# Kernel tuning notes

Hardware: AMD Instinct MI355X
Metric: run time of the kernel (lower is better)

The kernel has to match this reference:

```python
import jax, jax.numpy as jnp
import numpy as np


def setup_inputs() -> dict:
    key = jax.random.key(0)
    k1, k2 = jax.random.split(key)
    B, N, M = 8, 4096, 4096
    xyz1 = jax.random.normal(k1, (B, N, 3), dtype=jnp.float32)
    xyz2 = jax.random.normal(k2, (B, M, 3), dtype=jnp.float32)
    return {"xyz1": xyz1, "xyz2": xyz2}


def _chamfer_sq_dists(xyz1, xyz2):
    # Squared euclidean all-pairs distances via ||a||^2 + ||b||^2 - 2 a.b
    # xyz1: [B,N,3], xyz2: [B,M,3]
    n1 = jnp.sum(xyz1 * xyz1, axis=-1)              # [B,N]
    n2 = jnp.sum(xyz2 * xyz2, axis=-1)              # [B,M]
    dots = jnp.einsum('bnd,bmd->bnm', xyz1, xyz2)   # [B,N,M]
    d2 = n1[:, :, None] + n2[:, None, :] - 2.0 * dots
    dist1 = jnp.min(d2, axis=2)                     # [B,N] min over xyz2
    dist2 = jnp.min(d2, axis=1)                     # [B,M] min over xyz1
    return dist1, dist2


def reference(xyz1, xyz2):
    dist1, dist2 = _chamfer_sq_dists(xyz1, xyz2)
    return jnp.mean(dist1) + jnp.mean(dist2)
```

## Files before the change

kernel.cpp:

```cpp
#include <hip/hip_runtime.h>

typedef float f32x16 __attribute__((ext_vector_type(16)));
typedef short bf16x8 __attribute__((ext_vector_type(8)));

#define BLOCK 256
#define NPTS 4096
#define SEGS 32
#define CHUNK 256
#define NCHUNK (NPTS / CHUNK)
#define SUBS (CHUNK / 32)

__device__ inline unsigned int f2bf(float x) {
    unsigned int u = __float_as_uint(x);
    return (u + 0x7FFFu + ((u >> 16) & 1)) >> 16;
}
__device__ inline float bf2f(unsigned int b) { return __uint_as_float(b << 16); }
__device__ inline unsigned int pk2(unsigned int lo, unsigned int hi) {
    return (hi << 16) | (lo & 0xFFFFu);
}

__global__ __launch_bounds__(BLOCK) void chamfer_fused(
    const float* __restrict__ x1, const float* __restrict__ x2,
    int Bc, float inv1, float inv2, float* __restrict__ out) {
    __shared__ uint4 lds[2][2][CHUNK];
    __shared__ float wslot[128];
    __shared__ float red[4];

    int tid = threadIdx.x;
    int lane = tid & 63, widx = tid >> 6;
    int l31 = lane & 31, blk = lane >> 5;

    int bid = blockIdx.x;
    int seg = bid % SEGS;
    int bd = bid / SEGS;
    int dir = (bd >= Bc) ? 1 : 0;
    int b = dir ? bd - Bc : bd;
    const float* own = dir ? x2 : x1;
    const float* oth = dir ? x1 : x2;
    float inv = dir ? inv2 : inv1;

    int row0 = seg * 128 + widx * 32;

    bf16x8 afA;
    {
        const float* p = own + ((size_t)b * NPTS + row0 + l31) * 3;
        float x = p[0], y = p[1], z = p[2];
        float w = fmaf(z, z, fmaf(y, y, x * x));
        unsigned int hx = f2bf(x), hy = f2bf(y), hz = f2bf(z);
        unsigned int lx = f2bf(x - bf2f(hx)), ly = f2bf(y - bf2f(hy)), lz = f2bf(z - bf2f(hz));
        unsigned int ax = f2bf(-2.f * bf2f(hx)), ay = f2bf(-2.f * bf2f(hy)), az = f2bf(-2.f * bf2f(hz));
        unsigned int bx = f2bf(-2.f * bf2f(lx)), by = f2bf(-2.f * bf2f(ly)), bz = f2bf(-2.f * bf2f(lz));
        const unsigned int one = 0x3F80u;
        uint4 A0 = make_uint4(pk2(ax, ay), pk2(az, bx), pk2(by, bz), pk2(ax, ay));
        uint4 A1 = make_uint4(pk2(az, one), pk2(one, 0u), 0u, 0u);
        uint4 af4 = blk ? A1 : A0;
        afA = *(const bf16x8*)&af4;
        if (!blk) wslot[widx * 32 + l31] = w;
    }

    const float* os = oth + (size_t)b * NPTS * 3;
    {
        const float* q = os + (size_t)tid * 3;
        float x = q[0], y = q[1], z = q[2];
        float w = fmaf(z, z, fmaf(y, y, x * x));
        unsigned int hx = f2bf(x), hy = f2bf(y), hz = f2bf(z);
        unsigned int lx = f2bf(x - bf2f(hx)), ly = f2bf(y - bf2f(hy)), lz = f2bf(z - bf2f(hz));
        unsigned int hw = f2bf(w), lw = f2bf(w - bf2f(hw));
        lds[0][0][tid] = make_uint4(pk2(hx, hy), pk2(hz, hx), pk2(hy, hz), pk2(lx, ly));
        lds[0][1][tid] = make_uint4(pk2(lz, hw), pk2(lw, 0u), 0u, 0u);
    }
    __syncthreads();

    f32x16 run;
#pragma unroll
    for (int r = 0; r < 16; ++r) run[r] = 3.0e38f;

    f32x16 zero = {};
    for (int c = 0; c < NCHUNK; ++c) {
        int cur = c & 1;
        float nx, ny, nz;
        if (c + 1 < NCHUNK) {
            const float* q = os + (size_t)((c + 1) * CHUNK + tid) * 3;
            nx = q[0]; ny = q[1]; nz = q[2];
        }
        const uint4* lp = lds[cur][blk];
#pragma unroll
        for (int s = 0; s < SUBS; s += 2) {
            bf16x8 bf0 = *(const bf16x8*)(lp + s * 32 + l31);
            bf16x8 bf1 = *(const bf16x8*)(lp + (s + 1) * 32 + l31);
            f32x16 acc0 = __builtin_amdgcn_mfma_f32_32x32x16_bf16(afA, bf0, zero, 0, 0, 0);
            f32x16 acc1 = __builtin_amdgcn_mfma_f32_32x32x16_bf16(afA, bf1, zero, 0, 0, 0);
#pragma unroll
            for (int r = 0; r < 16; ++r)
                run[r] = fminf(run[r], fminf(acc0[r], acc1[r]));
        }
        if (c + 1 < NCHUNK) {
            float w = fmaf(nz, nz, fmaf(ny, ny, nx * nx));
            unsigned int hx = f2bf(nx), hy = f2bf(ny), hz = f2bf(nz);
            unsigned int lx = f2bf(nx - bf2f(hx)), ly = f2bf(ny - bf2f(hy)), lz = f2bf(nz - bf2f(hz));
            unsigned int hw = f2bf(w), lw = f2bf(w - bf2f(hw));
            lds[cur ^ 1][0][tid] = make_uint4(pk2(hx, hy), pk2(hz, hx), pk2(hy, hz), pk2(lx, ly));
            lds[cur ^ 1][1][tid] = make_uint4(pk2(lz, hw), pk2(lw, 0u), 0u, 0u);
        }
        __syncthreads();
    }

#pragma unroll
    for (int m = 1; m <= 16; m <<= 1)
#pragma unroll
        for (int r = 0; r < 16; ++r)
            run[r] = fminf(run[r], __shfl_xor(run[r], m, 64));

    float contrib = 0.0f;
    if (l31 == 0) {
#pragma unroll
        for (int r = 0; r < 16; ++r) {
            int lrow = (r & 3) + 8 * (r >> 2) + 4 * blk;
            contrib += run[r] + wslot[widx * 32 + lrow];
        }
    }
    contrib += __shfl_xor(contrib, 32, 64);
    if (lane == 0) red[widx] = contrib * inv;
    __syncthreads();
    if (tid == 0) atomicAdd(out, red[0] + red[1] + red[2] + red[3]);
}

__global__ __launch_bounds__(BLOCK) void chamfer_direct(
    const float* __restrict__ x1, const float* __restrict__ x2,
    int Npts, int Mpts, float inv1, float inv2, float* __restrict__ out) {
    int dir = blockIdx.z;
    const float* own = dir ? x2 : x1;
    const float* oth = dir ? x1 : x2;
    int np = dir ? Mpts : Npts;
    int mp = dir ? Npts : Mpts;
    float scale = dir ? inv2 : inv1;

    int bpb = np / BLOCK;
    int b = blockIdx.x / bpb;
    int i = (blockIdx.x % bpb) * BLOCK + threadIdx.x;

    const float* pp = own + ((size_t)b * np + i) * 3;
    float px = pp[0], py = pp[1], pz = pp[2];
    const float* o = oth + (size_t)b * mp * 3;

    float best = 3.0e38f;
#pragma unroll 4
    for (int j = 0; j < mp; ++j) {
        float dx = px - o[3 * j + 0];
        float dy = py - o[3 * j + 1];
        float dz = pz - o[3 * j + 2];
        float d2 = fmaf(dz, dz, fmaf(dy, dy, dx * dx));
        best = fminf(best, d2);
    }
    float s = best * scale;
    for (int off = 32; off; off >>= 1) s += __shfl_down(s, off, 64);
    __shared__ float red[BLOCK / 64];
    int lane = threadIdx.x & 63, wid = threadIdx.x >> 6;
    if (!lane) red[wid] = s;
    __syncthreads();
    if (!threadIdx.x) atomicAdd(out, red[0] + red[1] + red[2] + red[3]);
}

extern "C" void kernel_launch(void* const* d_in, const int* in_sizes, int n_in,
                              void* d_out, int out_size, void* d_ws, size_t ws_size,
                              hipStream_t stream) {
    const float* xyz1 = (const float*)d_in[0];
    const float* xyz2 = (const float*)d_in[1];
    float* out = (float*)d_out;

    const int Bc = in_sizes[0] / (3 * NPTS);
    const int n1 = Bc * NPTS;
    const int n2 = Bc * NPTS;
    bool okShape = Bc >= 1 && in_sizes[0] == Bc * 3 * NPTS && in_sizes[1] == in_sizes[0];

    hipMemsetAsync(d_out, 0, sizeof(float), stream);

    if (okShape) {
        chamfer_fused<<<Bc * 2 * SEGS, BLOCK, 0, stream>>>(
            xyz1, xyz2, Bc, 1.0f / (float)n1, 1.0f / (float)n2, out);
    } else {
        dim3 grid((in_sizes[0] / 3 / NPTS) * (NPTS / BLOCK), 1, 2);
        chamfer_direct<<<grid, BLOCK, 0, stream>>>(xyz1, xyz2, NPTS, NPTS,
                                                   1.0f / (float)n1, 1.0f / (float)n2, out);
    }
}
```

Before: 38.21 us.

## Precompute packed bf16 point fragments in a separate kernel and halve block size

Adds a pack kernel that converts every point once into hi/lo bf16 MFMA operand fragments and squared norms in workspace. It also zeroes the output, which replaces the memset. The main MFMA kernel then streams the prepacked B fragments straight into LDS instead of having every block redo the split-bf16 conversion for all 4096 points. Blocks shrink to 128 threads and twice as many segments run, so occupancy stays about the same while the grid grows. In exchange there is an extra kernel launch, and each block now reads about 32 bytes per point from L2 instead of 12.

```diff
diff --git a/kernel.cpp b/kernel.cpp
--- a/kernel.cpp
+++ b/kernel.cpp
@@ -3,9 +3,9 @@
 typedef float f32x16 __attribute__((ext_vector_type(16)));
 typedef short bf16x8 __attribute__((ext_vector_type(8)));
 
-#define BLOCK 256
+#define BLOCK 128
 #define NPTS 4096
-#define SEGS 32
+#define SEGS 64
 #define CHUNK 256
 #define NCHUNK (NPTS / CHUNK)
 #define SUBS (CHUNK / 32)
@@ -19,12 +19,38 @@
     return (hi << 16) | (lo & 0xFFFFu);
 }
 
-__global__ __launch_bounds__(BLOCK) void chamfer_fused(
+__global__ __launch_bounds__(256) void pack_pts(
     const float* __restrict__ x1, const float* __restrict__ x2,
-    int Bc, float inv1, float inv2, float* __restrict__ out) {
+    uint4* __restrict__ pA0, uint4* __restrict__ pA1,
+    uint4* __restrict__ pB0, uint4* __restrict__ pB1,
+    float* __restrict__ wn, int n1, int ntot, float* __restrict__ out) {
+    int i = blockIdx.x * 256 + threadIdx.x;
+    if (i == 0) out[0] = 0.0f;
+    if (i >= ntot) return;
+    const float* s = (i < n1) ? x1 + 3 * (size_t)i : x2 + 3 * (size_t)(i - n1);
+    float x = s[0], y = s[1], z = s[2];
+    float w = fmaf(z, z, fmaf(y, y, x * x));
+    wn[i] = w;
+    unsigned int hx = f2bf(x), hy = f2bf(y), hz = f2bf(z);
+    unsigned int lx = f2bf(x - bf2f(hx)), ly = f2bf(y - bf2f(hy)), lz = f2bf(z - bf2f(hz));
+    unsigned int hw = f2bf(w), lw = f2bf(w - bf2f(hw));
+    unsigned int ax = f2bf(-2.f * bf2f(hx)), ay = f2bf(-2.f * bf2f(hy)), az = f2bf(-2.f * bf2f(hz));
+    unsigned int bx = f2bf(-2.f * bf2f(lx)), by = f2bf(-2.f * bf2f(ly)), bz = f2bf(-2.f * bf2f(lz));
+    const unsigned int one = 0x3F80u;
+    pA0[i] = make_uint4(pk2(ax, ay), pk2(az, bx), pk2(by, bz), pk2(ax, ay));
+    pA1[i] = make_uint4(pk2(az, one), pk2(one, 0u), 0u, 0u);
+    pB0[i] = make_uint4(pk2(hx, hy), pk2(hz, hx), pk2(hy, hz), pk2(lx, ly));
+    pB1[i] = make_uint4(pk2(lz, hw), pk2(lw, 0u), 0u, 0u);
+}
+
+__global__ __launch_bounds__(BLOCK) void chamfer_mfma(
+    const uint4* __restrict__ pA0, const uint4* __restrict__ pA1,
+    const uint4* __restrict__ pB0, const uint4* __restrict__ pB1,
+    const float* __restrict__ wn, int n1, int Bc,
+    float inv1, float inv2, float* __restrict__ out) {
     __shared__ uint4 lds[2][2][CHUNK];
-    __shared__ float wslot[128];
-    __shared__ float red[4];
+    __shared__ float wslot[SEGS];
+    __shared__ float red[2];
 
     int tid = threadIdx.x;
     int lane = tid & 63, widx = tid >> 6;
@@ -35,40 +61,26 @@
     int bd = bid / SEGS;
     int dir = (bd >= Bc) ? 1 : 0;
     int b = dir ? bd - Bc : bd;
-    const float* own = dir ? x2 : x1;
-    const float* oth = dir ? x1 : x2;
+    int ownOff = dir ? n1 : 0;
+    int othOff = dir ? 0 : n1;
     float inv = dir ? inv2 : inv1;
 
-    int row0 = seg * 128 + widx * 32;
-
-    bf16x8 afA;
-    {
-        const float* p = own + ((size_t)b * NPTS + row0 + l31) * 3;
-        float x = p[0], y = p[1], z = p[2];
-        float w = fmaf(z, z, fmaf(y, y, x * x));
-        unsigned int hx = f2bf(x), hy = f2bf(y), hz = f2bf(z);
-        unsigned int lx = f2bf(x - bf2f(hx)), ly = f2bf(y - bf2f(hy)), lz = f2bf(z - bf2f(hz));
-        unsigned int ax = f2bf(-2.f * bf2f(hx)), ay = f2bf(-2.f * bf2f(hy)), az = f2bf(-2.f * bf2f(hz));
-        unsigned int bx = f2bf(-2.f * bf2f(lx)), by = f2bf(-2.f * bf2f(ly)), bz = f2bf(-2.f * bf2f(lz));
-        const unsigned int one = 0x3F80u;
-        uint4 A0 = make_uint4(pk2(ax, ay), pk2(az, bx), pk2(by, bz), pk2(ax, ay));
-        uint4 A1 = make_uint4(pk2(az, one), pk2(one, 0u), 0u, 0u);
-        uint4 af4 = blk ? A1 : A0;
-        afA = *(const bf16x8*)&af4;
-        if (!blk) wslot[widx * 32 + l31] = w;
-    }
-
-    const float* os = oth + (size_t)b * NPTS * 3;
-    {
-        const float* q = os + (size_t)tid * 3;
-        float x = q[0], y = q[1], z = q[2];
-        float w = fmaf(z, z, fmaf(y, y, x * x));
-        unsigned int hx = f2bf(x), hy = f2bf(y), hz = f2bf(z);
-        unsigned int lx = f2bf(x - bf2f(hx)), ly = f2bf(y - bf2f(hy)), lz = f2bf(z - bf2f(hz));
-        unsigned int hw = f2bf(w), lw = f2bf(w - bf2f(hw));
-        lds[0][0][tid] = make_uint4(pk2(hx, hy), pk2(hz, hx), pk2(hy, hz), pk2(lx, ly));
-        lds[0][1][tid] = make_uint4(pk2(lz, hw), pk2(lw, 0u), 0u, 0u);
-    }
+    int rowBase = seg * 64;
+    int row0 = rowBase + widx * 32;
+
+    size_t ownIdx = (size_t)(ownOff + b * NPTS + row0 + l31);
+    uint4 af4 = blk ? pA1[ownIdx] : pA0[ownIdx];
+    bf16x8 afA = *(const bf16x8*)&af4;
+
+    if (tid < SEGS) wslot[tid] = wn[ownOff + b * NPTS + rowBase + tid];
+
+    const uint4* gB0 = pB0 + (size_t)(othOff + b * NPTS);
+    const uint4* gB1 = pB1 + (size_t)(othOff + b * NPTS);
+
+    lds[0][0][tid]         = gB0[tid];
+    lds[0][0][tid + BLOCK] = gB0[tid + BLOCK];
+    lds[0][1][tid]         = gB1[tid];
+    lds[0][1][tid + BLOCK] = gB1[tid + BLOCK];
     __syncthreads();
 
     f32x16 run;
@@ -78,10 +90,11 @@
     f32x16 zero = {};
     for (int c = 0; c < NCHUNK; ++c) {
         int cur = c & 1;
-        float nx, ny, nz;
+        uint4 u00, u01, u10, u11;
         if (c + 1 < NCHUNK) {
-            const float* q = os + (size_t)((c + 1) * CHUNK + tid) * 3;
-            nx = q[0]; ny = q[1]; nz = q[2];
+            int off = (c + 1) * CHUNK;
+            u00 = gB0[off + tid]; u01 = gB0[off + tid + BLOCK];
+            u10 = gB1[off + tid]; u11 = gB1[off + tid + BLOCK];
         }
         const uint4* lp = lds[cur][blk];
 #pragma unroll
@@ -95,12 +108,10 @@
                 run[r] = fminf(run[r], fminf(acc0[r], acc1[r]));
         }
         if (c + 1 < NCHUNK) {
-            float w = fmaf(nz, nz, fmaf(ny, ny, nx * nx));
-            unsigned int hx = f2bf(nx), hy = f2bf(ny), hz = f2bf(nz);
-            unsigned int lx = f2bf(nx - bf2f(hx)), ly = f2bf(ny - bf2f(hy)), lz = f2bf(nz - bf2f(hz));
-            unsigned int hw = f2bf(w), lw = f2bf(w - bf2f(hw));
-            lds[cur ^ 1][0][tid] = make_uint4(pk2(hx, hy), pk2(hz, hx), pk2(hy, hz), pk2(lx, ly));
-            lds[cur ^ 1][1][tid] = make_uint4(pk2(lz, hw), pk2(lw, 0u), 0u, 0u);
+            lds[cur ^ 1][0][tid]         = u00;
+            lds[cur ^ 1][0][tid + BLOCK] = u01;
+            lds[cur ^ 1][1][tid]         = u10;
+            lds[cur ^ 1][1][tid + BLOCK] = u11;
         }
         __syncthreads();
     }
@@ -122,10 +133,10 @@
     contrib += __shfl_xor(contrib, 32, 64);
     if (lane == 0) red[widx] = contrib * inv;
     __syncthreads();
-    if (tid == 0) atomicAdd(out, red[0] + red[1] + red[2] + red[3]);
-}
-
-__global__ __launch_bounds__(BLOCK) void chamfer_direct(
+    if (tid == 0) atomicAdd(out, red[0] + red[1]);
+}
+
+__global__ __launch_bounds__(256) void chamfer_direct(
     const float* __restrict__ x1, const float* __restrict__ x2,
     int Npts, int Mpts, float inv1, float inv2, float* __restrict__ out) {
     int dir = blockIdx.z;
@@ -135,9 +146,9 @@
     int mp = dir ? Npts : Mpts;
     float scale = dir ? inv2 : inv1;
 
-    int bpb = np / BLOCK;
+    int bpb = np / 256;
     int b = blockIdx.x / bpb;
-    int i = (blockIdx.x % bpb) * BLOCK + threadIdx.x;
+    int i = (blockIdx.x % bpb) * 256 + threadIdx.x;
 
     const float* pp = own + ((size_t)b * np + i) * 3;
     float px = pp[0], py = pp[1], pz = pp[2];
@@ -154,7 +165,7 @@
     }
     float s = best * scale;
     for (int off = 32; off; off >>= 1) s += __shfl_down(s, off, 64);
-    __shared__ float red[BLOCK / 64];
+    __shared__ float red[4];
     int lane = threadIdx.x & 63, wid = threadIdx.x >> 6;
     if (!lane) red[wid] = s;
     __syncthreads();
@@ -171,16 +182,28 @@
     const int Bc = in_sizes[0] / (3 * NPTS);
     const int n1 = Bc * NPTS;
     const int n2 = Bc * NPTS;
+    const int ntot = n1 + n2;
+
+    size_t need = (size_t)ntot * (16 * 4 + 4);
     bool okShape = Bc >= 1 && in_sizes[0] == Bc * 3 * NPTS && in_sizes[1] == in_sizes[0];
 
-    hipMemsetAsync(d_out, 0, sizeof(float), stream);
-
-    if (okShape) {
-        chamfer_fused<<<Bc * 2 * SEGS, BLOCK, 0, stream>>>(
-            xyz1, xyz2, Bc, 1.0f / (float)n1, 1.0f / (float)n2, out);
+    if (okShape && ws_size >= need) {
+        uint4* pA0 = (uint4*)d_ws;
+        uint4* pA1 = pA0 + ntot;
+        uint4* pB0 = pA1 + ntot;
+        uint4* pB1 = pB0 + ntot;
+        float* wn = (float*)(pB1 + ntot);
+
+        pack_pts<<<(ntot + 255) / 256, 256, 0, stream>>>(
+            xyz1, xyz2, pA0, pA1, pB0, pB1, wn, n1, ntot, out);
+
+        chamfer_mfma<<<Bc * 2 * SEGS, BLOCK, 0, stream>>>(
+            pA0, pA1, pB0, pB1, wn, n1, Bc,
+            1.0f / (float)n1, 1.0f / (float)n2, out);
     } else {
-        dim3 grid((in_sizes[0] / 3 / NPTS) * (NPTS / BLOCK), 1, 2);
-        chamfer_direct<<<grid, BLOCK, 0, stream>>>(xyz1, xyz2, NPTS, NPTS,
-                                                   1.0f / (float)n1, 1.0f / (float)n2, out);
-    }
-}
+        hipMemsetAsync(d_out, 0, sizeof(float), stream);
+        dim3 grid((in_sizes[0] / 3 / NPTS) * (NPTS / 256), 1, 2);
+        chamfer_direct<<<grid, 256, 0, stream>>>(xyz1, xyz2, NPTS, NPTS,
+                                                 1.0f / (float)n1, 1.0f / (float)n2, out);
+    }
+}
```

Measured after the change: 42.79 us. 12.0% more time.
